# Kernel tuning notes

Measured on AMD Instinct MI355X. Metric: run time of the kernel, lower is better.

The kernel has to match this reference:

```python
import jax, jax.numpy as jnp
import numpy as np


def build_weights(target):
    """Vectorized version of the per-(batch,frame) distance-weight loop.

    target: [B, T, W, W]. For each frame, find the mean (row, col) coordinate
    of the maximal pixels, then weight = W / (dist_to_center + 1).
    """
    W = target.shape[-1]
    m = jnp.max(target, axis=(-2, -1), keepdims=True)
    mask = (target == m).astype(target.dtype)          # [B,T,W,W]
    cnt = jnp.sum(mask, axis=(-2, -1))                 # [B,T]
    idx = jnp.arange(W, dtype=target.dtype)            # [W]
    # mean row index x and mean col index y of argmax pixels
    x = jnp.sum(jnp.sum(mask, axis=-1) * idx, axis=-1) / cnt  # [B,T]
    y = jnp.sum(jnp.sum(mask, axis=-2) * idx, axis=-1) / cnt  # [B,T]
    a = idx[None, None, :, None] - x[:, :, None, None]  # row offsets [B,T,W,1]
    b = idx[None, None, None, :] - y[:, :, None, None]  # col offsets [B,T,1,W]
    dist = jnp.sqrt(a * a + b * b)                      # [B,T,W,W]
    return W / (dist + 1.0)  # reciprocal of (sqrt(dist)+1)/W


def setup_inputs() -> dict:
    key = jax.random.key(0)
    k1, k2 = jax.random.split(key)
    B, T, W = 16, 16, 256
    inp = jax.random.uniform(k1, (B, 1, T, W, W), dtype=jnp.float32)
    tgt = jax.random.uniform(k2, (B, T, W, W), dtype=jnp.float32)
    return {"input": inp, "target": tgt}


def reference(input, target):
    p = jnp.squeeze(input, axis=1)                 # [B,T,W,W]
    w = build_weights(target)
    # torch binary_cross_entropy clamps log terms at -100
    logp = jnp.clip(jnp.log(p), -100.0)
    log1mp = jnp.clip(jnp.log1p(-p), -100.0)
    loss = -jnp.mean(w * (target * logp + (1.0 - target) * log1mp))
    return loss
```

## Files before the change

### kernel.cpp

```cpp
#include <hip/hip_runtime.h>
#include <hip/hip_bf16.h>
#include <string.h>

#define WDIM 256
#define FRAME (WDIM * WDIM)
#define NFRAMES 256
#define NTOT ((long long)NFRAMES * FRAME)
#define BLOCK 1024


__device__ inline void monoid_merge(float& m, float& cnt, float& sr, float& sc,
                                    float m2, float cnt2, float sr2, float sc2) {
    if (m2 > m) { m = m2; cnt = cnt2; sr = sr2; sc = sc2; }
    else if (m2 == m) { cnt += cnt2; sr += sr2; sc += sc2; }
}

__device__ inline unsigned int pack_bf16x2(float a, float b) {
    __hip_bfloat162 h = __float22bfloat162_rn(make_float2(a, b));
    unsigned int u; memcpy(&u, &h, 4); return u;
}

__global__ __launch_bounds__(BLOCK, 4)
void floss_fused(const float* __restrict__ input, const float* __restrict__ target,
                 double* __restrict__ blocksum) {
    __shared__ unsigned int lds_t[FRAME / 2];
    __shared__ float sm[16], scnt[16], ssr[16], ssc[16];
    __shared__ float sx, sy;

    const int frame = blockIdx.x;
    const int tid = threadIdx.x;
    const int lane = tid & 63, wave = tid >> 6;

    const float4* __restrict__ t4 = (const float4*)(target + (size_t)frame * FRAME);
    const float4* __restrict__ p4 = (const float4*)(input  + (size_t)frame * FRAME);

    const float colb = (float)(lane * 4);
    float m = -1.0f, cnt = 0.0f, sr = 0.0f, sc = 0.0f;
    #pragma unroll
    for (int k = 0; k < 16; ++k) {
        const int i4 = k * 1024 + tid;
        const float4 v = t4[i4];
        const float row = (float)(16 * k + wave);
        const float vv[4] = {v.x, v.y, v.z, v.w};
        #pragma unroll
        for (int j = 0; j < 4; ++j) {
            const float val = vv[j];
            if (val > m)       { m = val; cnt = 1.0f; sr = row; sc = colb + (float)j; }
            else if (val == m) { cnt += 1.0f; sr += row; sc += colb + (float)j; }
        }
        *(uint2*)&lds_t[2 * i4] =
            make_uint2(pack_bf16x2(v.x, v.y), pack_bf16x2(v.z, v.w));
    }
    #pragma unroll
    for (int off = 32; off > 0; off >>= 1) {
        float m2  = __shfl_down(m, off);
        float c2  = __shfl_down(cnt, off);
        float sr2 = __shfl_down(sr, off);
        float sc2 = __shfl_down(sc, off);
        monoid_merge(m, cnt, sr, sc, m2, c2, sr2, sc2);
    }
    if (lane == 0) { sm[wave] = m; scnt[wave] = cnt; ssr[wave] = sr; ssc[wave] = sc; }
    __syncthreads();
    if (tid == 0) {
        m = sm[0]; cnt = scnt[0]; sr = ssr[0]; sc = ssc[0];
        #pragma unroll
        for (int w2 = 1; w2 < 16; ++w2)
            monoid_merge(m, cnt, sr, sc, sm[w2], scnt[w2], ssr[w2], ssc[w2]);
        const float rc = __builtin_amdgcn_rcpf(cnt);
        sx = sr * rc;
        sy = sc * rc;
    }
    __syncthreads();
    const float x = sx, y = sy;

    const float drb = (float)wave - x;
    float dc2[4];
    #pragma unroll
    for (int j = 0; j < 4; ++j) {
        const float d = colb + (float)j - y;
        dc2[j] = d * d;
    }

    float acc0 = 0.0f, acc1 = 0.0f;
    #pragma unroll
    for (int k = 0; k < 16; ++k) {
        const int i4 = k * 1024 + tid;
        const float4 pvv = p4[i4];
        const uint2 tw = *(const uint2*)&lds_t[2 * i4];
        const float tvv[4] = {
            __uint_as_float(tw.x << 16),
            __uint_as_float(tw.x & 0xffff0000u),
            __uint_as_float(tw.y << 16),
            __uint_as_float(tw.y & 0xffff0000u)
        };
        const float pp[4] = {pvv.x, pvv.y, pvv.z, pvv.w};
        const float dr = drb + (float)(16 * k);
        const float dr2 = dr * dr;
        #pragma unroll
        for (int j = 0; j < 4; ++j) {
            const float dist = __builtin_amdgcn_sqrtf(dr2 + dc2[j]);
            const float w = 256.0f * __builtin_amdgcn_rcpf(dist + 1.0f);
            const float p = pp[j];
            const float lp  = fmaxf(__logf(p), -100.0f);
            const float l1p = fmaxf(__logf(1.0f - p), -100.0f);
            if (j & 1) acc1 += w * fmaf(tvv[j], lp - l1p, l1p);
            else       acc0 += w * fmaf(tvv[j], lp - l1p, l1p);
        }
    }
    float local = acc0 + acc1;
    #pragma unroll
    for (int off = 32; off > 0; off >>= 1) local += __shfl_down(local, off);
    if (lane == 0) sm[wave] = local;
    __syncthreads();
    if (tid == 0) {
        float s = 0.0f;
        #pragma unroll
        for (int w2 = 0; w2 < 16; ++w2) s += sm[w2];
        blocksum[frame] = (double)s;
    }
}

__global__ __launch_bounds__(256)
void floss_final(const double* __restrict__ blocksum, float* __restrict__ out) {
    const int tid = threadIdx.x;
    const int lane = tid & 63, wave = tid >> 6;
    double v = blocksum[tid];
    #pragma unroll
    for (int off = 32; off > 0; off >>= 1) v += __shfl_down(v, off);
    __shared__ double sd[4];
    if (lane == 0) sd[wave] = v;
    __syncthreads();
    if (tid == 0)
        out[0] = (float)(-(sd[0] + sd[1] + sd[2] + sd[3]) / (double)NTOT);
}

extern "C" void kernel_launch(void* const* d_in, const int* in_sizes, int n_in,
                              void* d_out, int out_size, void* d_ws, size_t ws_size,
                              hipStream_t stream) {
    const float* input  = (const float*)d_in[0];
    const float* target = (const float*)d_in[1];
    float* out = (float*)d_out;
    double* blocksum = (double*)d_ws;

    floss_fused<<<NFRAMES, BLOCK, 0, stream>>>(input, target, blocksum);
    floss_final<<<1, 256, 0, stream>>>(blocksum, out);
}
```

Measured before the change: 148.6 us.

## Keep target in registers, split max and argmax-count passes, prefetch input

Each thread now holds its full target slice in 64 registers instead of packing it to bf16 in LDS, so the second pass reads exact fp32 target values with no shared-memory round trip. The argmax reduction is split into a plain max reduction followed by count, row and column sums taken only by threads that own the block max, merged through shared atomics. Input loads are double-buffered in groups of four float4 so global latency overlaps the log and sqrt work. The register footprint grows sharply (about 96 floats of buffered data per thread at 1024 threads), so spilling or lower occupancy is a risk, and the launch-bounds minimum-blocks hint is removed.

```diff
diff --git a/kernel.cpp b/kernel.cpp
--- a/kernel.cpp
+++ b/kernel.cpp
@@ -1,6 +1,4 @@
 #include <hip/hip_runtime.h>
-#include <hip/hip_bf16.h>
-#include <string.h>
 
 #define WDIM 256
 #define FRAME (WDIM * WDIM)
@@ -9,23 +7,12 @@
 #define BLOCK 1024
 
 
-__device__ inline void monoid_merge(float& m, float& cnt, float& sr, float& sc,
-                                    float m2, float cnt2, float sr2, float sc2) {
-    if (m2 > m) { m = m2; cnt = cnt2; sr = sr2; sc = sc2; }
-    else if (m2 == m) { cnt += cnt2; sr += sr2; sc += sc2; }
-}
-
-__device__ inline unsigned int pack_bf16x2(float a, float b) {
-    __hip_bfloat162 h = __float22bfloat162_rn(make_float2(a, b));
-    unsigned int u; memcpy(&u, &h, 4); return u;
-}
-
-__global__ __launch_bounds__(BLOCK, 4)
+__global__ __launch_bounds__(BLOCK)
 void floss_fused(const float* __restrict__ input, const float* __restrict__ target,
                  double* __restrict__ blocksum) {
-    __shared__ unsigned int lds_t[FRAME / 2];
-    __shared__ float sm[16], scnt[16], ssr[16], ssc[16];
-    __shared__ float sx, sy;
+    __shared__ float s_wmax[16];
+    __shared__ float s_cnt, s_sr, s_sc;
+    __shared__ float s_acc[16];
 
     const int frame = blockIdx.x;
     const int tid = threadIdx.x;
@@ -34,88 +21,100 @@
     const float4* __restrict__ t4 = (const float4*)(target + (size_t)frame * FRAME);
     const float4* __restrict__ p4 = (const float4*)(input  + (size_t)frame * FRAME);
 
-    const float colb = (float)(lane * 4);
-    float m = -1.0f, cnt = 0.0f, sr = 0.0f, sc = 0.0f;
+    if (tid == 0) { s_cnt = 0.0f; s_sr = 0.0f; s_sc = 0.0f; }
+
+    float4 tv[16];
     #pragma unroll
-    for (int k = 0; k < 16; ++k) {
-        const int i4 = k * 1024 + tid;
-        const float4 v = t4[i4];
-        const float row = (float)(16 * k + wave);
-        const float vv[4] = {v.x, v.y, v.z, v.w};
+    for (int k = 0; k < 16; ++k) tv[k] = t4[k * 1024 + tid];
+
+    float4 pva[4], pvb[4];
+    #pragma unroll
+    for (int k = 0; k < 4; ++k) pva[k] = p4[k * 1024 + tid];
+
+    float lmax = -1.0f;
+    #pragma unroll
+    for (int k = 0; k < 16; ++k)
+        lmax = fmaxf(lmax, fmaxf(fmaxf(tv[k].x, tv[k].y), fmaxf(tv[k].z, tv[k].w)));
+
+    float wmax = lmax;
+    #pragma unroll
+    for (int off = 32; off > 0; off >>= 1)
+        wmax = fmaxf(wmax, __shfl_down(wmax, off));
+    if (lane == 0) s_wmax[wave] = wmax;
+    __syncthreads();
+    float bmax = s_wmax[0];
+    #pragma unroll
+    for (int w2 = 1; w2 < 16; ++w2) bmax = fmaxf(bmax, s_wmax[w2]);
+
+    if (lmax == bmax) {
+        float cnt = 0.0f, sr = 0.0f, sc = 0.0f;
+        const float rowb = (float)wave;
+        const float colb = (float)(lane * 4);
         #pragma unroll
-        for (int j = 0; j < 4; ++j) {
-            const float val = vv[j];
-            if (val > m)       { m = val; cnt = 1.0f; sr = row; sc = colb + (float)j; }
-            else if (val == m) { cnt += 1.0f; sr += row; sc += colb + (float)j; }
+        for (int k = 0; k < 16; ++k) {
+            const float row = rowb + (float)(16 * k);
+            const float vv[4] = {tv[k].x, tv[k].y, tv[k].z, tv[k].w};
+            #pragma unroll
+            for (int j = 0; j < 4; ++j) {
+                if (vv[j] == bmax) { cnt += 1.0f; sr += row; sc += colb + (float)j; }
+            }
         }
-        *(uint2*)&lds_t[2 * i4] =
-            make_uint2(pack_bf16x2(v.x, v.y), pack_bf16x2(v.z, v.w));
-    }
-    #pragma unroll
-    for (int off = 32; off > 0; off >>= 1) {
-        float m2  = __shfl_down(m, off);
-        float c2  = __shfl_down(cnt, off);
-        float sr2 = __shfl_down(sr, off);
-        float sc2 = __shfl_down(sc, off);
-        monoid_merge(m, cnt, sr, sc, m2, c2, sr2, sc2);
-    }
-    if (lane == 0) { sm[wave] = m; scnt[wave] = cnt; ssr[wave] = sr; ssc[wave] = sc; }
-    __syncthreads();
-    if (tid == 0) {
-        m = sm[0]; cnt = scnt[0]; sr = ssr[0]; sc = ssc[0];
-        #pragma unroll
-        for (int w2 = 1; w2 < 16; ++w2)
-            monoid_merge(m, cnt, sr, sc, sm[w2], scnt[w2], ssr[w2], ssc[w2]);
-        const float rc = __builtin_amdgcn_rcpf(cnt);
-        sx = sr * rc;
-        sy = sc * rc;
+        atomicAdd(&s_cnt, cnt);
+        atomicAdd(&s_sr, sr);
+        atomicAdd(&s_sc, sc);
     }
     __syncthreads();
-    const float x = sx, y = sy;
+
+    const float rc = __builtin_amdgcn_rcpf(s_cnt);
+    const float x = s_sr * rc;
+    const float y = s_sc * rc;
 
     const float drb = (float)wave - x;
     float dc2[4];
     #pragma unroll
     for (int j = 0; j < 4; ++j) {
-        const float d = colb + (float)j - y;
+        const float d = (float)(lane * 4 + j) - y;
         dc2[j] = d * d;
     }
 
     float acc0 = 0.0f, acc1 = 0.0f;
     #pragma unroll
-    for (int k = 0; k < 16; ++k) {
-        const int i4 = k * 1024 + tid;
-        const float4 pvv = p4[i4];
-        const uint2 tw = *(const uint2*)&lds_t[2 * i4];
-        const float tvv[4] = {
-            __uint_as_float(tw.x << 16),
-            __uint_as_float(tw.x & 0xffff0000u),
-            __uint_as_float(tw.y << 16),
-            __uint_as_float(tw.y & 0xffff0000u)
-        };
-        const float pp[4] = {pvv.x, pvv.y, pvv.z, pvv.w};
-        const float dr = drb + (float)(16 * k);
-        const float dr2 = dr * dr;
+    for (int c = 0; c < 4; ++c) {
+        const float4* cur = (c & 1) ? pvb : pva;
+        float4* nxt = (c & 1) ? pva : pvb;
+        if (c < 3) {
+            #pragma unroll
+            for (int k2 = 0; k2 < 4; ++k2)
+                nxt[k2] = p4[((c + 1) * 4 + k2) * 1024 + tid];
+        }
         #pragma unroll
-        for (int j = 0; j < 4; ++j) {
-            const float dist = __builtin_amdgcn_sqrtf(dr2 + dc2[j]);
-            const float w = 256.0f * __builtin_amdgcn_rcpf(dist + 1.0f);
-            const float p = pp[j];
-            const float lp  = fmaxf(__logf(p), -100.0f);
-            const float l1p = fmaxf(__logf(1.0f - p), -100.0f);
-            if (j & 1) acc1 += w * fmaf(tvv[j], lp - l1p, l1p);
-            else       acc0 += w * fmaf(tvv[j], lp - l1p, l1p);
+        for (int k2 = 0; k2 < 4; ++k2) {
+            const int k = c * 4 + k2;
+            const float dr = drb + (float)(16 * k);
+            const float dr2 = dr * dr;
+            const float tt[4] = {tv[k].x, tv[k].y, tv[k].z, tv[k].w};
+            const float pp[4] = {cur[k2].x, cur[k2].y, cur[k2].z, cur[k2].w};
+            #pragma unroll
+            for (int j = 0; j < 4; ++j) {
+                const float dist = __builtin_amdgcn_sqrtf(dr2 + dc2[j]);
+                const float w = 256.0f * __builtin_amdgcn_rcpf(dist + 1.0f);
+                const float p = pp[j];
+                const float lp  = fmaxf(__logf(p), -100.0f);
+                const float l1p = fmaxf(__logf(1.0f - p), -100.0f);
+                if (j & 1) acc1 += w * fmaf(tt[j], lp - l1p, l1p);
+                else       acc0 += w * fmaf(tt[j], lp - l1p, l1p);
+            }
         }
     }
     float local = acc0 + acc1;
     #pragma unroll
     for (int off = 32; off > 0; off >>= 1) local += __shfl_down(local, off);
-    if (lane == 0) sm[wave] = local;
+    if (lane == 0) s_acc[wave] = local;
     __syncthreads();
     if (tid == 0) {
         float s = 0.0f;
         #pragma unroll
-        for (int w2 = 0; w2 < 16; ++w2) s += sm[w2];
+        for (int w2 = 0; w2 < 16; ++w2) s += s_acc[w2];
         blocksum[frame] = (double)s;
     }
 }
```

After: 148.8 us. No clear change (+0.2%).
